# Kernel tuning notes

Measured on AMD Instinct MI355X. Metric: run time of the kernel, lower is better.

## Reference

```python
import jax, jax.numpy as jnp
import numpy as np

B, G, K, N, M, E, L = 8, 512, 64, 1024, 128, 4, 5

def _lin(x, w, b):
    return x @ w.T + b

def setup_inputs():
    key = jax.random.key(0)
    ks = jax.random.split(key, 20)
    def nrm(k, shape, s=1.0):
        return jax.random.normal(k, shape, dtype=jnp.float32) * s
    def lin_p(k, out_d, in_d):
        k1, k2 = jax.random.split(k)
        s = 1.0 / float(np.sqrt(in_d))
        return nrm(k1, (out_d, in_d), s), nrm(k2, (out_d,), s)
    inp = {}
    inp["z"] = nrm(ks[0], (B, G, K, M), 0.5)
    inp["hs_grid"] = nrm(ks[1], (B, G, M))
    inp["hs_key"] = nrm(ks[2], (B, K, M))
    inp["lig_rep"] = nrm(ks[3], (B, E))
    inp["hs_rec"] = nrm(ks[4], (B, N, M))
    inp["w_Rl"] = jnp.ones((1,), dtype=jnp.float32)
    inp["w_mask"] = jax.random.randint(ks[5], (B, K), 0, 2)
    dims = {"wra": (M, M), "wrh": (M, M), "wla": (M, M), "wlh": (M, M),
            "z1": (1, M), "wcR": (M, M), "wcl": (M, M), "kR": (M, M),
            "mapL": (L, 2 * M + E), "fin": (1, L)}
    for i, nm in enumerate(dims):
        w, b = lin_p(ks[6 + i], *dims[nm])
        inp[nm + "_w"] = w
        inp[nm + "_b"] = b
    return inp

def reference(z, hs_grid, hs_key, lig_rep, hs_rec, w_Rl, w_mask,
              wra_w, wra_b, wrh_w, wrh_b, wla_w, wla_b, wlh_w, wlh_b,
              z1_w, z1_b, wcR_w, wcR_b, wcl_w, wcl_b, kR_w, kR_b,
              mapL_w, mapL_b, fin_w, fin_b):
    exp_z = jnp.exp(z)                                    # [B,G,K,M]
    zr = exp_z / exp_z.sum(axis=-2, keepdims=True)        # pseudo-softmax over K
    ra = jnp.einsum('bgkm,bkm->bgm', zr, hs_key)          # [B,G,M]
    zl = exp_z / exp_z.sum(axis=-3, keepdims=True)        # pseudo-softmax over G
    la = jnp.einsum('bgkm,bgm->bkm', zl, hs_grid)         # [B,K,M]
    ra_rh = _lin(ra, wra_w, wra_b) + _lin(hs_grid, wrh_w, wrh_b)  # [B,G,M]
    la_lh = _lin(la, wla_w, wla_b) + _lin(hs_key, wlh_w, wlh_b)   # [B,K,M]
    att = _lin(z, z1_w, z1_b)[..., 0]                     # [B,G,K]
    att_l = jax.nn.softmax(att, axis=2).sum(axis=1)       # [B,K]
    att_r = jax.nn.softmax(att, axis=1).sum(axis=2)       # [B,G]
    key_rep = jnp.einsum('bk,bkm->bm', att_l, la_lh)      # [B,M]
    grid_rep = jnp.einsum('bg,bgm->bm', att_r, ra_rh)     # [B,M]
    Rh = _lin(hs_rec, wcR_w, wcR_b)                       # [B,N,M]
    lh = _lin(hs_key, wcl_w, wcl_b)                       # [B,K,M]
    z_Rl = jnp.einsum('bnh,bkh->bnk', Rh, lh)             # [B,N,K]
    masked = jnp.where(w_mask[:, None, :] == 0, jnp.float32(-1e10), w_Rl * z_Rl)
    z_Rl = jax.nn.softmax(masked, axis=1)                 # softmax over N
    kfr = jnp.einsum('bnk,bnh->bkh', z_Rl, hs_rec)        # [B,K,M]
    kfr = _lin(kfr, kR_w, kR_b)
    kfr = jnp.einsum('bk,bkh->bh', att_l, kfr)            # [B,M]
    key_rep = key_rep + kfr
    pair_rep = jnp.concatenate([key_rep, lig_rep, grid_rep], axis=1)  # [B,2M+E]
    pair_rep = _lin(pair_rep, mapL_w, mapL_b)             # [B,L]
    return _lin(pair_rep, fin_w, fin_b)[..., 0]           # [B]
```

## Files before the change

### kernel.cpp

```cpp
#include <hip/hip_runtime.h>

#define Bb 8
#define Gg 512
#define Kk 64
#define Nn 1024
#define Mm 128
#define KM (Kk * Mm)
#define GPB 8
#define NCH (Gg / GPB)

struct P7 { const float* p[7]; };

__global__ __launch_bounds__(1024) void kA(
    const float* __restrict__ z, const float* __restrict__ hs_grid,
    const float* __restrict__ hs_key, const float* __restrict__ z1w,
    P7 ptrs, float* __restrict__ wT,
    float* __restrict__ raOut, float* __restrict__ attOut,
    float* __restrict__ laNum, float* __restrict__ laDen)
{
  __shared__ __align__(16) float smem[17408];
  const int bid = blockIdx.x;
  const int t = threadIdx.x;

  if (bid >= Bb * NCH) {
    float* tile = smem;
    const int r = bid - Bb * NCH;
    const int mat = r >> 4, tl = r & 15;
    const int xo = (tl & 3) * 32, y0 = (tl >> 2) * 32;
    const int tx = t & 31, ty = t >> 5;
    const float* src = ptrs.p[mat];
    float* dst = wT + (size_t)mat * Mm * Mm;
    tile[ty * 33 + tx] = src[(size_t)(y0 + ty) * Mm + xo + tx];
    __syncthreads();
    dst[(size_t)(xo + ty) * Mm + y0 + tx] = tile[tx * 33 + ty];
    return;
  }

  float* s_hskey  = smem;
  float* s_hsgrid = smem + 8192;
  float* s_rn     = smem + 9216;
  float* s_rd     = smem + 13312;

  const int b = bid >> 6;
  const int gblk = bid & 63;
  const int lane_m = t & 31;
  const int m4 = lane_m << 2;
  const int kgrp = t >> 5;
  const int wv = t >> 6;

  const float* hkb = hs_key + (size_t)b * KM;
  for (int idx = t; idx < KM; idx += 1024) s_hskey[idx] = hkb[idx];
  const float* hgb = hs_grid + ((size_t)b * Gg + gblk * GPB) * Mm;
  for (int idx = t; idx < GPB * Mm; idx += 1024) s_hsgrid[idx] = hgb[idx];

  const float zw0 = z1w[m4], zw1 = z1w[m4 + 1], zw2 = z1w[m4 + 2], zw3 = z1w[m4 + 3];

  float la_n[2][4], la_d[2][4];
#pragma unroll
  for (int i = 0; i < 2; ++i)
#pragma unroll
    for (int j = 0; j < 4; ++j) { la_n[i][j] = 0.f; la_d[i][j] = 0.f; }

  const float* zb = z + ((size_t)b * Gg + gblk * GPB) * (size_t)Mm * Kk;
  const int ofs0 = (kgrp * 2) * Mm + m4;
  const int ofs1 = ofs0 + Mm;
  float4 c0 = *reinterpret_cast<const float4*>(zb + ofs0);
  float4 c1 = *reinterpret_cast<const float4*>(zb + ofs1);

  __syncthreads();

  for (int gl = 0; gl < GPB; ++gl) {
    float4 n0 = c0, n1 = c1;
    if (gl < GPB - 1) {
      n0 = *reinterpret_cast<const float4*>(zb + (size_t)(gl + 1) * KM + ofs0);
      n1 = *reinterpret_cast<const float4*>(zb + (size_t)(gl + 1) * KM + ofs1);
    }
    const int g = gblk * GPB + gl;
    const float4 hg = *reinterpret_cast<const float4*>(s_hsgrid + gl * Mm + m4);
    float rn0 = 0, rn1 = 0, rn2 = 0, rn3 = 0, rd0 = 0, rd1 = 0, rd2 = 0, rd3 = 0;
#pragma unroll
    for (int i = 0; i < 2; ++i) {
      const float4 v = (i == 0) ? c0 : c1;
      const int k = kgrp * 2 + i;
      const float e0 = __expf(v.x), e1 = __expf(v.y), e2 = __expf(v.z), e3 = __expf(v.w);
      la_n[i][0] += e0 * hg.x; la_n[i][1] += e1 * hg.y; la_n[i][2] += e2 * hg.z; la_n[i][3] += e3 * hg.w;
      la_d[i][0] += e0;        la_d[i][1] += e1;        la_d[i][2] += e2;        la_d[i][3] += e3;
      const float4 hk = *reinterpret_cast<const float4*>(s_hskey + k * Mm + m4);
      rn0 += e0 * hk.x; rn1 += e1 * hk.y; rn2 += e2 * hk.z; rn3 += e3 * hk.w;
      rd0 += e0; rd1 += e1; rd2 += e2; rd3 += e3;
      float ap = v.x * zw0 + v.y * zw1 + v.z * zw2 + v.w * zw3;
      ap += __shfl_xor(ap, 16); ap += __shfl_xor(ap, 8); ap += __shfl_xor(ap, 4);
      ap += __shfl_xor(ap, 2);  ap += __shfl_xor(ap, 1);
      if (lane_m == 0) attOut[((size_t)b * Gg + g) * Kk + k] = ap;
    }
    rn0 += __shfl_xor(rn0, 32); rn1 += __shfl_xor(rn1, 32); rn2 += __shfl_xor(rn2, 32); rn3 += __shfl_xor(rn3, 32);
    rd0 += __shfl_xor(rd0, 32); rd1 += __shfl_xor(rd1, 32); rd2 += __shfl_xor(rd2, 32); rd3 += __shfl_xor(rd3, 32);
    float* rnB = s_rn + (gl & 1) * 2048;
    float* rdB = s_rd + (gl & 1) * 2048;
    if ((t & 63) < 32) {
      *reinterpret_cast<float4*>(rnB + wv * Mm + m4) = make_float4(rn0, rn1, rn2, rn3);
      *reinterpret_cast<float4*>(rdB + wv * Mm + m4) = make_float4(rd0, rd1, rd2, rd3);
    }
    __syncthreads();
    if (t < Mm) {
      float num = 0.f, den = 0.f;
#pragma unroll
      for (int ww = 0; ww < 16; ++ww) { num += rnB[ww * Mm + t]; den += rdB[ww * Mm + t]; }
      raOut[((size_t)b * Gg + g) * Mm + t] = num / den;
    }
    c0 = n0; c1 = n1;
  }

  const size_t base = ((size_t)(b * NCH + gblk)) * KM;
#pragma unroll
  for (int i = 0; i < 2; ++i) {
    const int k = kgrp * 2 + i;
    *reinterpret_cast<float4*>(laNum + base + k * Mm + m4) =
        make_float4(la_n[i][0], la_n[i][1], la_n[i][2], la_n[i][3]);
    *reinterpret_cast<float4*>(laDen + base + k * Mm + m4) =
        make_float4(la_d[i][0], la_d[i][1], la_d[i][2], la_d[i][3]);
  }
}

__device__ __forceinline__ void lin2_body(
    int r0, const float* __restrict__ in1, const float* __restrict__ W1T,
    const float* __restrict__ in2, const float* __restrict__ W2T,
    const float* __restrict__ b1, const float* __restrict__ b2,
    float* __restrict__ out, float* smem)
{
  float* s1 = smem;
  float* s2 = smem + 2048;
  float* sacc = smem + 4096;
  const int t = threadIdx.x;
  const int m = t & 127, hh = t >> 7;
  for (int idx = t; idx < 2048; idx += 256) s1[idx] = in1[(size_t)r0 * Mm + idx];
  if (in2) for (int idx = t; idx < 2048; idx += 256) s2[idx] = in2[(size_t)r0 * Mm + idx];
  __syncthreads();
  float acc[16];
#pragma unroll
  for (int r = 0; r < 16; ++r) acc[r] = 0.f;
  const int h0 = hh * 64;
  if (in2) {
    for (int h = h0; h < h0 + 64; ++h) {
      const float w1 = W1T[(size_t)h * Mm + m];
      const float w2 = W2T[(size_t)h * Mm + m];
#pragma unroll
      for (int r = 0; r < 16; ++r) acc[r] += s1[r * Mm + h] * w1 + s2[r * Mm + h] * w2;
    }
  } else {
    for (int h = h0; h < h0 + 64; ++h) {
      const float w1 = W1T[(size_t)h * Mm + m];
#pragma unroll
      for (int r = 0; r < 16; ++r) acc[r] += s1[r * Mm + h] * w1;
    }
  }
  if (hh == 1) {
#pragma unroll
    for (int r = 0; r < 16; ++r) sacc[r * Mm + m] = acc[r];
  }
  __syncthreads();
  if (hh == 0) {
    const float bias = b1[m] + (b2 ? b2[m] : 0.f);
#pragma unroll
    for (int r = 0; r < 16; ++r) out[(size_t)(r0 + r) * Mm + m] = acc[r] + sacc[r * Mm + m] + bias;
  }
}

__global__ __launch_bounds__(256) void kB(
    const float* __restrict__ laNum, const float* __restrict__ laDen, float* __restrict__ la,
    const float* __restrict__ att, float* __restrict__ attlP,
    float* __restrict__ attrPM, float* __restrict__ attrPS,
    const float* __restrict__ hs_rec, const float* __restrict__ hs_key,
    const float* __restrict__ wT, const float* __restrict__ wcR_b, const float* __restrict__ wcl_b,
    float* __restrict__ Rh, float* __restrict__ lh)
{
  __shared__ __align__(16) float smem[6144];
  const int bid = blockIdx.x;
  const int t = threadIdx.x;

  if (bid < 256) {
    const int idx = bid * 256 + t;
    const int b = idx >> 13, r = idx & 8191;
    const float* np = laNum + (size_t)b * NCH * KM + r;
    const float* dp = laDen + (size_t)b * NCH * KM + r;
    float num = 0.f, den = 0.f;
#pragma unroll 8
    for (int p = 0; p < NCH; ++p) { num += np[(size_t)p * KM]; den += dp[(size_t)p * KM]; }
    la[idx] = num / den;
  } else if (bid < 320) {
    const int blk = bid - 256;
    const int b = blk >> 3, p = blk & 7;
    const int w = t >> 6, lane = t & 63;
    float acc = 0.f;
    for (int j = 0; j < 16; ++j) {
      const int g = p * 64 + w * 16 + j;
      const float a = att[((size_t)b * Gg + g) * Kk + lane];
      float mx = a;
      for (int off = 32; off; off >>= 1) mx = fmaxf(mx, __shfl_xor(mx, off));
      const float e = __expf(a - mx);
      float s = e;
      for (int off = 32; off; off >>= 1) s += __shfl_xor(s, off);
      acc += e / s;
    }
    float* sred = smem;
    sred[w * 64 + lane] = acc;
    __syncthreads();
    if (t < 64) attlP[(b * 8 + p) * 64 + t] = sred[t] + sred[64 + t] + sred[128 + t] + sred[192 + t];
  } else if (bid < 384) {
    const int blk = bid - 320;
    const int b = blk >> 3, gc = blk & 7;
    const int k = t & 63, j4 = t >> 6;
    float m = -1e30f, s = 0.f;
    for (int j = 0; j < 16; ++j) {
      const int g = gc * 64 + j4 * 16 + j;
      const float a = att[((size_t)b * Gg + g) * Kk + k];
      if (a > m) { s = s * __expf(m - a) + 1.0f; m = a; }
      else s += __expf(a - m);
    }
    float* sm = smem;
    float* ss = smem + 256;
    sm[j4 * 64 + k] = m; ss[j4 * 64 + k] = s;
    __syncthreads();
    if (t < 64) {
      float M = sm[t];
      for (int q = 1; q < 4; ++q) M = fmaxf(M, sm[q * 64 + t]);
      float S = 0.f;
      for (int q = 0; q < 4; ++q) S += ss[q * 64 + t] * __expf(sm[q * 64 + t] - M);
      attrPM[(b * 8 + gc) * 64 + t] = M;
      attrPS[(b * 8 + gc) * 64 + t] = S;
    }
  } else if (bid < 896) {
    lin2_body((bid - 384) * 16, hs_rec, wT + 4 * 16384, nullptr, nullptr, wcR_b, nullptr, Rh, smem);
  } else {
    lin2_body((bid - 896) * 16, hs_key, wT + 5 * 16384, nullptr, nullptr, wcl_b, nullptr, lh, smem);
  }
}

__global__ __launch_bounds__(256) void kC(
    const float* __restrict__ att, const float* __restrict__ attrPM, const float* __restrict__ attrPS,
    float* __restrict__ att_r,
    const float* __restrict__ ra, const float* __restrict__ hs_grid,
    const float* __restrict__ la, const float* __restrict__ hs_key,
    const float* __restrict__ wT,
    const float* __restrict__ wra_b, const float* __restrict__ wrh_b,
    const float* __restrict__ wla_b, const float* __restrict__ wlh_b,
    float* __restrict__ ra_rh, float* __restrict__ la_lh,
    const float* __restrict__ Rh, const float* __restrict__ lh,
    const int* __restrict__ mask, const float* __restrict__ wRl,
    float* __restrict__ scores, float* __restrict__ pmT, float* __restrict__ psT)
{
  __shared__ __align__(16) float smem[14912];
  const int bid = blockIdx.x;
  const int t = threadIdx.x;

  if (bid < 64) {
    const int b = bid >> 3, gc = bid & 7;
    const int k = t & 63, grp = t >> 6;
    float* Mx = smem;
    float* S = smem + 64;
    if (t < 64) {
      float M = -1e30f;
      for (int p = 0; p < 8; ++p) M = fmaxf(M, attrPM[(b * 8 + p) * 64 + t]);
      float s = 0.f;
      for (int p = 0; p < 8; ++p) s += attrPS[(b * 8 + p) * 64 + t] * __expf(attrPM[(b * 8 + p) * 64 + t] - M);
      Mx[t] = M; S[t] = s;
    }
    __syncthreads();
    const float Mk = Mx[k], Sk = S[k];
    for (int j = 0; j < 16; ++j) {
      const int g = gc * 64 + grp * 16 + j;
      float p = __expf(att[((size_t)b * Gg + g) * Kk + k] - Mk) / Sk;
      for (int off = 32; off; off >>= 1) p += __shfl_xor(p, off);
      if (k == 0) att_r[b * Gg + g] = p;
    }
  } else if (bid < 320) {
    lin2_body((bid - 64) * 16, ra, wT, hs_grid, wT + 16384, wra_b, wrh_b, ra_rh, smem);
  } else if (bid < 352) {
    lin2_body((bid - 320) * 16, la, wT + 2 * 16384, hs_key, wT + 3 * 16384, wla_b, wlh_b, la_lh, smem);
  } else {
    const int vb = bid - 352;
    const int b = vb >> 6, ntile = vb & 63;
    const int n0 = ntile * 16;
    const int k = t & 63, hs = t >> 6;
    float* s_rh  = smem;
    float* s_lh  = smem + 2048;
    float* s_acc = smem + 10304;
    float* s_m   = smem + 14400;
    float* s_s   = smem + 14656;
    for (int idx = t; idx < 2048; idx += 256)
      s_rh[idx] = Rh[((size_t)b * Nn + n0) * Mm + idx];
    for (int idx = t; idx < 8192; idx += 256)
      s_lh[(idx >> 7) * 129 + (idx & 127)] = lh[(size_t)b * Kk * Mm + idx];
    __syncthreads();
    float acc[16];
#pragma unroll
    for (int r = 0; r < 16; ++r) acc[r] = 0.f;
    for (int h = hs * 32; h < hs * 32 + 32; ++h) {
      const float lv = s_lh[k * 129 + h];
#pragma unroll
      for (int r = 0; r < 16; ++r) acc[r] += s_rh[r * Mm + h] * lv;
    }
#pragma unroll
    for (int r = 0; r < 16; ++r) s_acc[(hs * 16 + r) * 64 + k] = acc[r];
    __syncthreads();
    const float wv = wRl[0];
    const bool msk = (mask[b * Kk + k] == 0);
    float m = -3.0e38f, ssum = 0.f;
    for (int q = 0; q < 4; ++q) {
      const int idx = q * 256 + t;
      const int r = idx >> 6, kk = idx & 63;
      float v = s_acc[r * 64 + kk] + s_acc[(16 + r) * 64 + kk] +
                s_acc[(32 + r) * 64 + kk] + s_acc[(48 + r) * 64 + kk];
      v = msk ? -1e10f : wv * v;
      scores[((size_t)b * Nn + n0 + r) * Kk + kk] = v;
      if (v > m) { ssum = ssum * __expf(m - v) + 1.0f; m = v; }
      else ssum += __expf(v - m);
    }
    s_m[hs * 64 + k] = m; s_s[hs * 64 + k] = ssum;
    __syncthreads();
    if (t < 64) {
      float M = fmaxf(fmaxf(s_m[t], s_m[64 + t]), fmaxf(s_m[128 + t], s_m[192 + t]));
      float S = 0.f;
#pragma unroll
      for (int q = 0; q < 4; ++q) S += s_s[q * 64 + t] * __expf(s_m[q * 64 + t] - M);
      pmT[((size_t)b * 64 + ntile) * 64 + t] = M;
      psT[((size_t)b * 64 + ntile) * 64 + t] = S;
    }
  }
}

__global__ __launch_bounds__(512) void kD(
    const float* __restrict__ scores, const float* __restrict__ hs_rec,
    const float* __restrict__ pmT, const float* __restrict__ psT,
    float* __restrict__ kfrP)
{
  __shared__ float sP[2048];
  __shared__ float sM[64], sS[64], sFm[8], sFs[8];
  const int b = blockIdx.x >> 5;
  const int k8 = (blockIdx.x >> 2) & 7;
  const int ns = blockIdx.x & 3;
  const int t = threadIdx.x;
  const int h = t & 127, kq = t >> 7;
  const int n0 = ns * 256;

  if (t < 64) {
    const int kk = t & 7, ch = t >> 3;
    const int kg = k8 * 8 + kk;
    float m = -3.0e38f, s = 0.f;
    for (int nt = ch * 8; nt < ch * 8 + 8; ++nt) {
      const float pm = pmT[((size_t)b * 64 + nt) * 64 + kg];
      const float ps = psT[((size_t)b * 64 + nt) * 64 + kg];
      if (pm > m) { s = s * __expf(m - pm) + ps; m = pm; }
      else s += ps * __expf(pm - m);
    }
    sM[t] = m; sS[t] = s;
  }
  __syncthreads();
  if (t < 8) {
    float M = -3.0e38f;
    for (int ch = 0; ch < 8; ++ch) M = fmaxf(M, sM[ch * 8 + t]);
    float S = 0.f;
    for (int ch = 0; ch < 8; ++ch) S += sS[ch * 8 + t] * __expf(sM[ch * 8 + t] - M);
    sFm[t] = M; sFs[t] = 1.0f / S;
  }
  __syncthreads();

  {
    const float* sc = scores + ((size_t)b * Nn + n0) * Kk + k8 * 8;
    for (int idx = t; idx < 2048; idx += 512) {
      const int n = idx >> 3, kk = idx & 7;
      sP[n * 8 + kk] = __expf(sc[(size_t)n * Kk + kk] - sFm[kk]) * sFs[kk];
    }
  }
  __syncthreads();
  const int kk0 = kq * 2;
  float a0 = 0.f, a1 = 0.f;
  const float* hr = hs_rec + ((size_t)b * Nn + n0) * Mm + h;
  for (int n = 0; n < 256; ++n) {
    const float hv = hr[(size_t)n * Mm];
    a0 += sP[n * 8 + kk0] * hv;
    a1 += sP[n * 8 + kk0 + 1] * hv;
  }
  const int k0 = k8 * 8 + kk0;
  kfrP[(((size_t)b * 4 + ns) * Kk + k0) * Mm + h] = a0;
  kfrP[(((size_t)b * 4 + ns) * Kk + k0 + 1) * Mm + h] = a1;
}

__global__ __launch_bounds__(1024) void kE(
    const float* __restrict__ attl_part, const float* __restrict__ att_r,
    const float* __restrict__ la_lh, const float* __restrict__ kfrP,
    const float* __restrict__ kRT, const float* __restrict__ kR_b,
    const float* __restrict__ ra_rh, const float* __restrict__ lig_rep,
    const float* __restrict__ mapL_w, const float* __restrict__ mapL_b,
    const float* __restrict__ fin_w, const float* __restrict__ fin_b,
    float* __restrict__ out)
{
  const int b = blockIdx.x;
  const int t = threadIdx.x;
  const int h = t & 127, sg = t >> 7;
  __shared__ float s_attl[64];
  __shared__ float s_attr[Gg];
  __shared__ float s_pair[264];
  __shared__ float s_u[Mm];
  __shared__ float s_red[8][Mm];
  __shared__ float s5[16];

  if (t < 64) {
    float a = 0.f;
    for (int p = 0; p < 8; ++p) a += attl_part[(b * 8 + p) * 64 + t];
    s_attl[t] = a;
  }
  if (t < Gg) s_attr[t] = att_r[b * Gg + t];
  __syncthreads();

  {
    float acc = 0.f;
    for (int j = 0; j < 8; ++j) {
      const int k = sg * 8 + j;
      acc += s_attl[k] * la_lh[((size_t)b * Kk + k) * Mm + h];
    }
    s_red[sg][h] = acc;
  }
  __syncthreads();
  if (sg == 0) {
    float v = 0.f;
#pragma unroll
    for (int q = 0; q < 8; ++q) v += s_red[q][h];
    s_pair[h] = v;
  }
  __syncthreads();

  {
    float acc = 0.f;
    for (int j = 0; j < 32; ++j) {
      const int row = sg * 32 + j;
      acc += s_attl[row & 63] * kfrP[((size_t)b * 256 + row) * Mm + h];
    }
    s_red[sg][h] = acc;
  }
  __syncthreads();
  if (sg == 0) {
    float v = 0.f;
#pragma unroll
    for (int q = 0; q < 8; ++q) v += s_red[q][h];
    s_u[h] = v;
  }
  __syncthreads();

  {
    float acc = 0.f;
    for (int j = 0; j < 16; ++j) {
      const int hp = sg * 16 + j;
      acc += s_u[hp] * kRT[(size_t)hp * Mm + h];
    }
    s_red[sg][h] = acc;
  }
  __syncthreads();
  if (sg == 0) {
    float sA = 0.f;
    for (int k2 = 0; k2 < 64; ++k2) sA += s_attl[k2];
    float v = 0.f;
#pragma unroll
    for (int q = 0; q < 8; ++q) v += s_red[q][h];
    s_pair[h] += v + sA * kR_b[h];
  }
  __syncthreads();

  {
    float acc = 0.f;
    for (int j = 0; j < 64; ++j) {
      const int g = sg * 64 + j;
      acc += s_attr[g] * ra_rh[((size_t)b * Gg + g) * Mm + h];
    }
    s_red[sg][h] = acc;
  }
  __syncthreads();
  if (sg == 0) {
    float v = 0.f;
#pragma unroll
    for (int q = 0; q < 8; ++q) v += s_red[q][h];
    s_pair[132 + h] = v;
  }
  if (t < 4) s_pair[128 + t] = lig_rep[b * 4 + t];
  __syncthreads();

  const int l = t >> 6, lane = t & 63;
  if (l < 5) {
    float acc = 0.f;
    for (int c = lane; c < 260; c += 64) acc += s_pair[c] * mapL_w[l * 260 + c];
    for (int off = 32; off; off >>= 1) acc += __shfl_xor(acc, off);
    if (lane == 0) s5[l] = acc + mapL_b[l];
  }
  __syncthreads();
  if (t == 0) {
    float o = fin_b[0];
    for (int l2 = 0; l2 < 5; ++l2) o += s5[l2] * fin_w[l2];
    out[b] = o;
  }
}

extern "C" void kernel_launch(void* const* d_in, const int* in_sizes, int n_in,
                              void* d_out, int out_size, void* d_ws, size_t ws_size,
                              hipStream_t stream) {
  const float* z       = (const float*)d_in[0];
  const float* hs_grid = (const float*)d_in[1];
  const float* hs_key  = (const float*)d_in[2];
  const float* lig_rep = (const float*)d_in[3];
  const float* hs_rec  = (const float*)d_in[4];
  const float* w_Rl    = (const float*)d_in[5];
  const int*   w_mask  = (const int*)d_in[6];
  const float* wra_w = (const float*)d_in[7];  const float* wra_b = (const float*)d_in[8];
  const float* wrh_w = (const float*)d_in[9];  const float* wrh_b = (const float*)d_in[10];
  const float* wla_w = (const float*)d_in[11]; const float* wla_b = (const float*)d_in[12];
  const float* wlh_w = (const float*)d_in[13]; const float* wlh_b = (const float*)d_in[14];
  const float* z1_w  = (const float*)d_in[15];
  const float* wcR_w = (const float*)d_in[17]; const float* wcR_b = (const float*)d_in[18];
  const float* wcl_w = (const float*)d_in[19]; const float* wcl_b = (const float*)d_in[20];
  const float* kR_w  = (const float*)d_in[21]; const float* kR_b  = (const float*)d_in[22];
  const float* mapL_w = (const float*)d_in[23]; const float* mapL_b = (const float*)d_in[24];
  const float* fin_w  = (const float*)d_in[25]; const float* fin_b  = (const float*)d_in[26];
  float* out = (float*)d_out;

  float* w = (float*)d_ws;
  float* wT    = w;
  float* ra    = wT + 7 * 16384;
  float* att   = ra + Bb * Gg * Mm;
  float* laNum = att + Bb * Gg * Kk;
  float* laDen = laNum + Bb * NCH * Kk * Mm;
  float* la    = laDen + Bb * NCH * Kk * Mm;
  float* attlP = la + Bb * Kk * Mm;
  float* attrPM = attlP + Bb * 8 * 64;
  float* attrPS = attrPM + Bb * 8 * 64;
  float* att_r = attrPS + Bb * 8 * 64;
  float* ra_rh = att_r + Bb * Gg;
  float* la_lh = ra_rh + Bb * Gg * Mm;
  float* Rh    = la_lh + Bb * Kk * Mm;
  float* lh    = Rh + Bb * Nn * Mm;
  float* scores = lh + Bb * Kk * Mm;

  float* pmT  = laNum;
  float* psT  = laNum + 32768;
  float* kfrP = laDen;

  P7 ptrs;
  ptrs.p[0] = wra_w; ptrs.p[1] = wrh_w; ptrs.p[2] = wla_w; ptrs.p[3] = wlh_w;
  ptrs.p[4] = wcR_w; ptrs.p[5] = wcl_w; ptrs.p[6] = kR_w;

  kA<<<Bb * NCH + 112, 1024, 0, stream>>>(z, hs_grid, hs_key, z1_w, ptrs, wT,
                                          ra, att, laNum, laDen);
  kB<<<928, 256, 0, stream>>>(laNum, laDen, la, att, attlP, attrPM, attrPS,
                              hs_rec, hs_key, wT, wcR_b, wcl_b, Rh, lh);
  kC<<<864, 256, 0, stream>>>(att, attrPM, attrPS, att_r, ra, hs_grid, la, hs_key,
                              wT, wra_b, wrh_b, wla_b, wlh_b, ra_rh, la_lh,
                              Rh, lh, w_mask, w_Rl, scores, pmT, psT);
  kD<<<Bb * 8 * 4, 512, 0, stream>>>(scores, hs_rec, pmT, psT, kfrP);
  kE<<<Bb, 1024, 0, stream>>>(attlP, att_r, la_lh, kfrP, wT + 6 * 16384, kR_b,
                              ra_rh, lig_rep, mapL_w, mapL_b, fin_w, fin_b, out);
}
```

Before: 99.76 us.

## Reassociate weighted sums before linear layers and double grid rows per block

Linear maps are moved after the attention-weighted reductions, using sum_g a_g(W x_g + b) = W(sum_g a_g x_g) + (sum a)·b. The full ra_rh and la_lh matrices are no longer materialised; only reduced vectors are multiplied by the weights in the final kernel. The kfr path is rearranged the same way: att_l is folded into the softmax probabilities, leaving one weighted vector over hs_rec per batch. GPB also rises from 8 to 16, which halves the number of partial la chunks kB must sum, though kA gets fewer blocks.

```diff
diff --git a/kernel.cpp b/kernel.cpp
--- a/kernel.cpp
+++ b/kernel.cpp
@@ -6,7 +6,7 @@
 #define Nn 1024
 #define Mm 128
 #define KM (Kk * Mm)
-#define GPB 8
+#define GPB 16
 #define NCH (Gg / GPB)
 
 struct P7 { const float* p[7]; };
@@ -18,7 +18,7 @@
     float* __restrict__ raOut, float* __restrict__ attOut,
     float* __restrict__ laNum, float* __restrict__ laDen)
 {
-  __shared__ __align__(16) float smem[17408];
+  __shared__ __align__(16) float smem[18432];
   const int bid = blockIdx.x;
   const int t = threadIdx.x;
 
@@ -38,11 +38,11 @@
 
   float* s_hskey  = smem;
   float* s_hsgrid = smem + 8192;
-  float* s_rn     = smem + 9216;
-  float* s_rd     = smem + 13312;
-
-  const int b = bid >> 6;
-  const int gblk = bid & 63;
+  float* s_rn     = smem + 10240;
+  float* s_rd     = smem + 14336;
+
+  const int b = bid >> 5;
+  const int gblk = bid & 31;
   const int lane_m = t & 31;
   const int m4 = lane_m << 2;
   const int kgrp = t >> 5;
@@ -122,37 +122,24 @@
   }
 }
 
-__device__ __forceinline__ void lin2_body(
+__device__ __forceinline__ void lin1_body(
     int r0, const float* __restrict__ in1, const float* __restrict__ W1T,
-    const float* __restrict__ in2, const float* __restrict__ W2T,
-    const float* __restrict__ b1, const float* __restrict__ b2,
-    float* __restrict__ out, float* smem)
+    const float* __restrict__ b1, float* __restrict__ out, float* smem)
 {
   float* s1 = smem;
-  float* s2 = smem + 2048;
-  float* sacc = smem + 4096;
+  float* sacc = smem + 2048;
   const int t = threadIdx.x;
   const int m = t & 127, hh = t >> 7;
   for (int idx = t; idx < 2048; idx += 256) s1[idx] = in1[(size_t)r0 * Mm + idx];
-  if (in2) for (int idx = t; idx < 2048; idx += 256) s2[idx] = in2[(size_t)r0 * Mm + idx];
   __syncthreads();
   float acc[16];
 #pragma unroll
   for (int r = 0; r < 16; ++r) acc[r] = 0.f;
   const int h0 = hh * 64;
-  if (in2) {
-    for (int h = h0; h < h0 + 64; ++h) {
-      const float w1 = W1T[(size_t)h * Mm + m];
-      const float w2 = W2T[(size_t)h * Mm + m];
-#pragma unroll
-      for (int r = 0; r < 16; ++r) acc[r] += s1[r * Mm + h] * w1 + s2[r * Mm + h] * w2;
-    }
-  } else {
-    for (int h = h0; h < h0 + 64; ++h) {
-      const float w1 = W1T[(size_t)h * Mm + m];
-#pragma unroll
-      for (int r = 0; r < 16; ++r) acc[r] += s1[r * Mm + h] * w1;
-    }
+  for (int h = h0; h < h0 + 64; ++h) {
+    const float w1 = W1T[(size_t)h * Mm + m];
+#pragma unroll
+    for (int r = 0; r < 16; ++r) acc[r] += s1[r * Mm + h] * w1;
   }
   if (hh == 1) {
 #pragma unroll
@@ -160,7 +147,7 @@
   }
   __syncthreads();
   if (hh == 0) {
-    const float bias = b1[m] + (b2 ? b2[m] : 0.f);
+    const float bias = b1[m];
 #pragma unroll
     for (int r = 0; r < 16; ++r) out[(size_t)(r0 + r) * Mm + m] = acc[r] + sacc[r * Mm + m] + bias;
   }
@@ -174,7 +161,7 @@
     const float* __restrict__ wT, const float* __restrict__ wcR_b, const float* __restrict__ wcl_b,
     float* __restrict__ Rh, float* __restrict__ lh)
 {
-  __shared__ __align__(16) float smem[6144];
+  __shared__ __align__(16) float smem[4096];
   const int bid = blockIdx.x;
   const int t = threadIdx.x;
 
@@ -230,21 +217,15 @@
       attrPS[(b * 8 + gc) * 64 + t] = S;
     }
   } else if (bid < 896) {
-    lin2_body((bid - 384) * 16, hs_rec, wT + 4 * 16384, nullptr, nullptr, wcR_b, nullptr, Rh, smem);
+    lin1_body((bid - 384) * 16, hs_rec, wT + 4 * 16384, wcR_b, Rh, smem);
   } else {
-    lin2_body((bid - 896) * 16, hs_key, wT + 5 * 16384, nullptr, nullptr, wcl_b, nullptr, lh, smem);
+    lin1_body((bid - 896) * 16, hs_key, wT + 5 * 16384, wcl_b, lh, smem);
   }
 }
 
 __global__ __launch_bounds__(256) void kC(
     const float* __restrict__ att, const float* __restrict__ attrPM, const float* __restrict__ attrPS,
     float* __restrict__ att_r,
-    const float* __restrict__ ra, const float* __restrict__ hs_grid,
-    const float* __restrict__ la, const float* __restrict__ hs_key,
-    const float* __restrict__ wT,
-    const float* __restrict__ wra_b, const float* __restrict__ wrh_b,
-    const float* __restrict__ wla_b, const float* __restrict__ wlh_b,
-    float* __restrict__ ra_rh, float* __restrict__ la_lh,
     const float* __restrict__ Rh, const float* __restrict__ lh,
     const int* __restrict__ mask, const float* __restrict__ wRl,
     float* __restrict__ scores, float* __restrict__ pmT, float* __restrict__ psT)
@@ -273,12 +254,8 @@
       for (int off = 32; off; off >>= 1) p += __shfl_xor(p, off);
       if (k == 0) att_r[b * Gg + g] = p;
     }
-  } else if (bid < 320) {
-    lin2_body((bid - 64) * 16, ra, wT, hs_grid, wT + 16384, wra_b, wrh_b, ra_rh, smem);
-  } else if (bid < 352) {
-    lin2_body((bid - 320) * 16, la, wT + 2 * 16384, hs_key, wT + 3 * 16384, wla_b, wlh_b, la_lh, smem);
   } else {
-    const int vb = bid - 352;
+    const int vb = bid - 64;
     const int b = vb >> 6, ntile = vb & 63;
     const int n0 = ntile * 16;
     const int k = t & 63, hs = t >> 6;
@@ -332,169 +309,183 @@
 __global__ __launch_bounds__(512) void kD(
     const float* __restrict__ scores, const float* __restrict__ hs_rec,
     const float* __restrict__ pmT, const float* __restrict__ psT,
-    float* __restrict__ kfrP)
+    const float* __restrict__ attlP, const float* __restrict__ att_r,
+    const float* __restrict__ ra, const float* __restrict__ hs_grid,
+    const float* __restrict__ la, const float* __restrict__ hs_key,
+    float* __restrict__ uP, float* __restrict__ w1P, float* __restrict__ w2P,
+    float* __restrict__ w0P, float* __restrict__ v1, float* __restrict__ v2,
+    float* __restrict__ sAv)
 {
-  __shared__ float sP[2048];
-  __shared__ float sM[64], sS[64], sFm[8], sFs[8];
-  const int b = blockIdx.x >> 5;
-  const int k8 = (blockIdx.x >> 2) & 7;
-  const int ns = blockIdx.x & 3;
+  __shared__ float sm[1280];
+  __shared__ float s_attl[64];
+  __shared__ float sM[64], sSi[64];
+  const int bid = blockIdx.x;
   const int t = threadIdx.x;
-  const int h = t & 127, kq = t >> 7;
-  const int n0 = ns * 256;
-
-  if (t < 64) {
-    const int kk = t & 7, ch = t >> 3;
-    const int kg = k8 * 8 + kk;
-    float m = -3.0e38f, s = 0.f;
-    for (int nt = ch * 8; nt < ch * 8 + 8; ++nt) {
-      const float pm = pmT[((size_t)b * 64 + nt) * 64 + kg];
-      const float ps = psT[((size_t)b * 64 + nt) * 64 + kg];
-      if (pm > m) { s = s * __expf(m - pm) + ps; m = pm; }
-      else s += ps * __expf(pm - m);
-    }
-    sM[t] = m; sS[t] = s;
-  }
-  __syncthreads();
-  if (t < 8) {
-    float M = -3.0e38f;
-    for (int ch = 0; ch < 8; ++ch) M = fmaxf(M, sM[ch * 8 + t]);
-    float S = 0.f;
-    for (int ch = 0; ch < 8; ++ch) S += sS[ch * 8 + t] * __expf(sM[ch * 8 + t] - M);
-    sFm[t] = M; sFs[t] = 1.0f / S;
-  }
-  __syncthreads();
-
-  {
-    const float* sc = scores + ((size_t)b * Nn + n0) * Kk + k8 * 8;
-    for (int idx = t; idx < 2048; idx += 512) {
-      const int n = idx >> 3, kk = idx & 7;
-      sP[n * 8 + kk] = __expf(sc[(size_t)n * Kk + kk] - sFm[kk]) * sFs[kk];
-    }
-  }
-  __syncthreads();
-  const int kk0 = kq * 2;
-  float a0 = 0.f, a1 = 0.f;
-  const float* hr = hs_rec + ((size_t)b * Nn + n0) * Mm + h;
-  for (int n = 0; n < 256; ++n) {
-    const float hv = hr[(size_t)n * Mm];
-    a0 += sP[n * 8 + kk0] * hv;
-    a1 += sP[n * 8 + kk0 + 1] * hv;
-  }
-  const int k0 = k8 * 8 + kk0;
-  kfrP[(((size_t)b * 4 + ns) * Kk + k0) * Mm + h] = a0;
-  kfrP[(((size_t)b * 4 + ns) * Kk + k0 + 1) * Mm + h] = a1;
-}
-
-__global__ __launch_bounds__(1024) void kE(
-    const float* __restrict__ attl_part, const float* __restrict__ att_r,
-    const float* __restrict__ la_lh, const float* __restrict__ kfrP,
-    const float* __restrict__ kRT, const float* __restrict__ kR_b,
-    const float* __restrict__ ra_rh, const float* __restrict__ lig_rep,
+
+  if (bid < 64) {
+    const int b = bid >> 3, nc = bid & 7;
+    if (t < 64) {
+      float a = 0.f;
+      for (int p = 0; p < 8; ++p) a += attlP[(b * 8 + p) * 64 + t];
+      s_attl[t] = a;
+      float M = -3.0e38f;
+      for (int nt = 0; nt < 64; ++nt) M = fmaxf(M, pmT[((size_t)b * 64 + nt) * 64 + t]);
+      float S = 0.f;
+      for (int nt = 0; nt < 64; ++nt)
+        S += psT[((size_t)b * 64 + nt) * 64 + t] * __expf(pmT[((size_t)b * 64 + nt) * 64 + t] - M);
+      sM[t] = M; sSi[t] = 1.0f / S;
+    }
+    __syncthreads();
+    const int n = t >> 2, ks = t & 3;
+    const float* sc = scores + ((size_t)b * Nn + nc * 128 + n) * Kk + ks * 16;
+    float qp = 0.f;
+#pragma unroll
+    for (int j = 0; j < 16; ++j) {
+      const int k = ks * 16 + j;
+      qp += s_attl[k] * __expf(sc[j] - sM[k]) * sSi[k];
+    }
+    sm[n * 4 + ks] = qp;
+    __syncthreads();
+    float* q = sm + 512;
+    if (t < 128) q[t] = sm[t * 4] + sm[t * 4 + 1] + sm[t * 4 + 2] + sm[t * 4 + 3];
+    __syncthreads();
+    const int h = t & 127, nq = t >> 7;
+    float acc = 0.f;
+    const float* hr = hs_rec + ((size_t)b * Nn + nc * 128 + nq * 32) * Mm + h;
+    for (int j = 0; j < 32; ++j) acc += q[nq * 32 + j] * hr[(size_t)j * Mm];
+    float* red = sm + 640;
+    red[nq * 128 + h] = acc;
+    __syncthreads();
+    if (t < 128) uP[((size_t)b * 8 + nc) * 128 + t] = red[t] + red[128 + t] + red[256 + t] + red[384 + t];
+  } else if (bid < 128) {
+    const int blk = bid - 64;
+    const int b = blk >> 3, gc = blk & 7;
+    float* s_ar = sm + 1152;
+    if (t < 64) s_ar[t] = att_r[b * Gg + gc * 64 + t];
+    __syncthreads();
+    const int h = t & 127, gq = t >> 7;
+    float a1 = 0.f, a2 = 0.f;
+    const float* rp = ra + ((size_t)b * Gg + gc * 64 + gq * 16) * Mm + h;
+    const float* gp = hs_grid + ((size_t)b * Gg + gc * 64 + gq * 16) * Mm + h;
+    for (int j = 0; j < 16; ++j) {
+      const float w = s_ar[gq * 16 + j];
+      a1 += w * rp[(size_t)j * Mm];
+      a2 += w * gp[(size_t)j * Mm];
+    }
+    float* r1 = sm;
+    float* r2 = sm + 512;
+    r1[gq * 128 + h] = a1; r2[gq * 128 + h] = a2;
+    __syncthreads();
+    if (t < 128) {
+      w1P[((size_t)b * 8 + gc) * 128 + t] = r1[t] + r1[128 + t] + r1[256 + t] + r1[384 + t];
+      w2P[((size_t)b * 8 + gc) * 128 + t] = r2[t] + r2[128 + t] + r2[256 + t] + r2[384 + t];
+    }
+    if (t == 0) {
+      float s = 0.f;
+      for (int j = 0; j < 64; ++j) s += s_ar[j];
+      w0P[b * 8 + gc] = s;
+    }
+  } else {
+    const int b = bid - 128;
+    if (t < 64) {
+      float a = 0.f;
+      for (int p = 0; p < 8; ++p) a += attlP[(b * 8 + p) * 64 + t];
+      s_attl[t] = a;
+    }
+    __syncthreads();
+    const int h = t & 127, kq = t >> 7;
+    float a1 = 0.f, a2 = 0.f;
+    const float* lp = la + ((size_t)b * Kk + kq * 16) * Mm + h;
+    const float* kp = hs_key + ((size_t)b * Kk + kq * 16) * Mm + h;
+    for (int j = 0; j < 16; ++j) {
+      const float w = s_attl[kq * 16 + j];
+      a1 += w * lp[(size_t)j * Mm];
+      a2 += w * kp[(size_t)j * Mm];
+    }
+    float* r1 = sm;
+    float* r2 = sm + 512;
+    r1[kq * 128 + h] = a1; r2[kq * 128 + h] = a2;
+    __syncthreads();
+    if (t < 128) {
+      v1[b * 128 + t] = r1[t] + r1[128 + t] + r1[256 + t] + r1[384 + t];
+      v2[b * 128 + t] = r2[t] + r2[128 + t] + r2[256 + t] + r2[384 + t];
+    }
+    if (t == 0) {
+      float s = 0.f;
+      for (int j = 0; j < 64; ++j) s += s_attl[j];
+      sAv[b] = s;
+    }
+  }
+}
+
+__global__ __launch_bounds__(256) void kE(
+    const float* __restrict__ uP, const float* __restrict__ w1P, const float* __restrict__ w2P,
+    const float* __restrict__ w0P, const float* __restrict__ v1, const float* __restrict__ v2,
+    const float* __restrict__ sAv, const float* __restrict__ wT,
+    const float* __restrict__ wra_b, const float* __restrict__ wrh_b,
+    const float* __restrict__ wla_b, const float* __restrict__ wlh_b,
+    const float* __restrict__ kR_b, const float* __restrict__ lig_rep,
     const float* __restrict__ mapL_w, const float* __restrict__ mapL_b,
     const float* __restrict__ fin_w, const float* __restrict__ fin_b,
     float* __restrict__ out)
 {
-  const int b = blockIdx.x;
-  const int t = threadIdx.x;
-  const int h = t & 127, sg = t >> 7;
-  __shared__ float s_attl[64];
-  __shared__ float s_attr[Gg];
-  __shared__ float s_pair[264];
-  __shared__ float s_u[Mm];
-  __shared__ float s_red[8][Mm];
-  __shared__ float s5[16];
-
-  if (t < 64) {
-    float a = 0.f;
-    for (int p = 0; p < 8; ++p) a += attl_part[(b * 8 + p) * 64 + t];
-    s_attl[t] = a;
-  }
-  if (t < Gg) s_attr[t] = att_r[b * Gg + t];
-  __syncthreads();
-
-  {
+  __shared__ float sV1[128], sV2[128], sU[128], sW1[128], sW2[128];
+  __shared__ float sPair[260];
+  __shared__ float sRed[2][2][128];
+  __shared__ float s5[8];
+  __shared__ float sSc[2];
+  const int b = blockIdx.x, t = threadIdx.x;
+  const int m = t & 127, hf = t >> 7;
+
+  if (t < 128) {
+    float u = 0.f, w1 = 0.f, w2 = 0.f;
+    for (int c = 0; c < 8; ++c) {
+      u  += uP[((size_t)b * 8 + c) * 128 + t];
+      w1 += w1P[((size_t)b * 8 + c) * 128 + t];
+      w2 += w2P[((size_t)b * 8 + c) * 128 + t];
+    }
+    sU[t] = u; sW1[t] = w1; sW2[t] = w2;
+    sV1[t] = v1[b * 128 + t]; sV2[t] = v2[b * 128 + t];
+  }
+  if (t == 0) {
+    float s = 0.f;
+    for (int c = 0; c < 8; ++c) s += w0P[b * 8 + c];
+    sSc[0] = s;
+    sSc[1] = sAv[b];
+  }
+  __syncthreads();
+
+  const float* wraT = wT;
+  const float* wrhT = wT + 1 * 16384;
+  const float* wlaT = wT + 2 * 16384;
+  const float* wlhT = wT + 3 * 16384;
+  const float* kRT  = wT + 6 * 16384;
+  float key = 0.f, grd = 0.f;
+  for (int h = hf * 64; h < hf * 64 + 64; ++h) {
+    key += sV1[h] * wlaT[h * Mm + m] + sV2[h] * wlhT[h * Mm + m] + sU[h] * kRT[h * Mm + m];
+    grd += sW1[h] * wraT[h * Mm + m] + sW2[h] * wrhT[h * Mm + m];
+  }
+  sRed[0][hf][m] = key; sRed[1][hf][m] = grd;
+  __syncthreads();
+  if (t < 128) {
+    const float sR = sSc[0], sA = sSc[1];
+    sPair[t] = sRed[0][0][t] + sRed[0][1][t] + sA * (wla_b[t] + wlh_b[t] + kR_b[t]);
+    sPair[132 + t] = sRed[1][0][t] + sRed[1][1][t] + sR * (wra_b[t] + wrh_b[t]);
+  }
+  if (t < 4) sPair[128 + t] = lig_rep[b * 4 + t];
+  __syncthreads();
+
+  const int wv = t >> 6, lane = t & 63;
+  for (int l = wv; l < 5; l += 4) {
     float acc = 0.f;
-    for (int j = 0; j < 8; ++j) {
-      const int k = sg * 8 + j;
-      acc += s_attl[k] * la_lh[((size_t)b * Kk + k) * Mm + h];
-    }
-    s_red[sg][h] = acc;
-  }
-  __syncthreads();
-  if (sg == 0) {
-    float v = 0.f;
-#pragma unroll
-    for (int q = 0; q < 8; ++q) v += s_red[q][h];
-    s_pair[h] = v;
-  }
-  __syncthreads();
-
-  {
-    float acc = 0.f;
-    for (int j = 0; j < 32; ++j) {
-      const int row = sg * 32 + j;
-      acc += s_attl[row & 63] * kfrP[((size_t)b * 256 + row) * Mm + h];
-    }
-    s_red[sg][h] = acc;
-  }
-  __syncthreads();
-  if (sg == 0) {
-    float v = 0.f;
-#pragma unroll
-    for (int q = 0; q < 8; ++q) v += s_red[q][h];
-    s_u[h] = v;
-  }
-  __syncthreads();
-
-  {
-    float acc = 0.f;
-    for (int j = 0; j < 16; ++j) {
-      const int hp = sg * 16 + j;
-      acc += s_u[hp] * kRT[(size_t)hp * Mm + h];
-    }
-    s_red[sg][h] = acc;
-  }
-  __syncthreads();
-  if (sg == 0) {
-    float sA = 0.f;
-    for (int k2 = 0; k2 < 64; ++k2) sA += s_attl[k2];
-    float v = 0.f;
-#pragma unroll
-    for (int q = 0; q < 8; ++q) v += s_red[q][h];
-    s_pair[h] += v + sA * kR_b[h];
-  }
-  __syncthreads();
-
-  {
-    float acc = 0.f;
-    for (int j = 0; j < 64; ++j) {
-      const int g = sg * 64 + j;
-      acc += s_attr[g] * ra_rh[((size_t)b * Gg + g) * Mm + h];
-    }
-    s_red[sg][h] = acc;
-  }
-  __syncthreads();
-  if (sg == 0) {
-    float v = 0.f;
-#pragma unroll
-    for (int q = 0; q < 8; ++q) v += s_red[q][h];
-    s_pair[132 + h] = v;
-  }
-  if (t < 4) s_pair[128 + t] = lig_rep[b * 4 + t];
-  __syncthreads();
-
-  const int l = t >> 6, lane = t & 63;
-  if (l < 5) {
-    float acc = 0.f;
-    for (int c = lane; c < 260; c += 64) acc += s_pair[c] * mapL_w[l * 260 + c];
+    for (int c = lane; c < 260; c += 64) acc += sPair[c] * mapL_w[l * 260 + c];
     for (int off = 32; off; off >>= 1) acc += __shfl_xor(acc, off);
     if (lane == 0) s5[l] = acc + mapL_b[l];
   }
   __syncthreads();
   if (t == 0) {
     float o = fin_b[0];
-    for (int l2 = 0; l2 < 5; ++l2) o += s5[l2] * fin_w[l2];
+    for (int l = 0; l < 5; ++l) o += s5[l] * fin_w[l];
     out[b] = o;
   }
 }
@@ -532,15 +523,19 @@
   float* attrPM = attlP + Bb * 8 * 64;
   float* attrPS = attrPM + Bb * 8 * 64;
   float* att_r = attrPS + Bb * 8 * 64;
-  float* ra_rh = att_r + Bb * Gg;
-  float* la_lh = ra_rh + Bb * Gg * Mm;
-  float* Rh    = la_lh + Bb * Kk * Mm;
+  float* Rh    = att_r + Bb * Gg;
   float* lh    = Rh + Bb * Nn * Mm;
   float* scores = lh + Bb * Kk * Mm;
 
   float* pmT  = laNum;
   float* psT  = laNum + 32768;
-  float* kfrP = laDen;
+  float* uP   = laNum + 65536;
+  float* w1P  = laNum + 73728;
+  float* w2P  = laNum + 81920;
+  float* w0P  = laNum + 90112;
+  float* v1   = laNum + 90176;
+  float* v2   = laNum + 91200;
+  float* sAv  = laNum + 92224;
 
   P7 ptrs;
   ptrs.p[0] = wra_w; ptrs.p[1] = wrh_w; ptrs.p[2] = wla_w; ptrs.p[3] = wlh_w;
@@ -550,10 +545,12 @@
                                           ra, att, laNum, laDen);
   kB<<<928, 256, 0, stream>>>(laNum, laDen, la, att, attlP, attrPM, attrPS,
                               hs_rec, hs_key, wT, wcR_b, wcl_b, Rh, lh);
-  kC<<<864, 256, 0, stream>>>(att, attrPM, attrPS, att_r, ra, hs_grid, la, hs_key,
-                              wT, wra_b, wrh_b, wla_b, wlh_b, ra_rh, la_lh,
-                              Rh, lh, w_mask, w_Rl, scores, pmT, psT);
-  kD<<<Bb * 8 * 4, 512, 0, stream>>>(scores, hs_rec, pmT, psT, kfrP);
-  kE<<<Bb, 1024, 0, stream>>>(attlP, att_r, la_lh, kfrP, wT + 6 * 16384, kR_b,
-                              ra_rh, lig_rep, mapL_w, mapL_b, fin_w, fin_b, out);
-}
+  kC<<<576, 256, 0, stream>>>(att, attrPM, attrPS, att_r, Rh, lh,
+                              w_mask, w_Rl, scores, pmT, psT);
+  kD<<<136, 512, 0, stream>>>(scores, hs_rec, pmT, psT, attlP, att_r,
+                              ra, hs_grid, la, hs_key,
+                              uP, w1P, w2P, w0P, v1, v2, sAv);
+  kE<<<Bb, 256, 0, stream>>>(uP, w1P, w2P, w0P, v1, v2, sAv, wT,
+                             wra_b, wrh_b, wla_b, wlh_b, kR_b, lig_rep,
+                             mapL_w, mapL_b, fin_w, fin_b, out);
+}
```

Measured after the change: 89.20 us. 1.12x faster.
